# Kernel tuning notes

Hardware: AMD Instinct MI355X
Metric: run time of the kernel (lower is better)

Reference implementation:

```python
import jax, jax.numpy as jnp
import numpy as np

DIM = 1024
R = 2                      # upscale_factor
D_MODEL = DIM // (R * R)   # 256
D_INNER = 2 * D_MODEL      # expand=2 -> 512
D_STATE = 16
D_CONV = 4
DT_RANK = (D_MODEL + 15) // 16  # 16
NUM_TOKENS = 1


def pixel_shuffle(x, r):
    # (B, C*r^2, H, W) -> (B, C, H*r, W*r)
    B, C, H, W = x.shape
    c = C // (r * r)
    x = x.reshape(B, c, r, r, H, W)
    x = x.transpose(0, 1, 4, 2, 5, 3)
    return x.reshape(B, c, H * r, W * r)


def pixel_unshuffle(x, r):
    # (B, C, H*r, W*r) -> (B, C*r^2, H, W)
    B, C, Hr, Wr = x.shape
    H, W = Hr // r, Wr // r
    x = x.reshape(B, C, H, r, W, r)
    x = x.transpose(0, 1, 3, 5, 2, 4)
    return x.reshape(B, C * r * r, H, W)


def setup_inputs() -> dict:
    key = jax.random.key(0)
    ks = jax.random.split(key, 12)
    s = lambda k, shape, scale=0.02: jax.random.normal(k, shape, dtype=jnp.float32) * scale
    inp = {
        "x": jax.random.normal(ks[0], (4, DIM, 24, 24), dtype=jnp.float32),
        "global_token": jnp.zeros((1, NUM_TOKENS, D_MODEL), dtype=jnp.float32),
        "in_proj_w": s(ks[1], (2 * D_INNER, D_MODEL)),
        "conv_w": s(ks[2], (D_INNER, D_CONV), 0.1),
        "conv_b": jnp.zeros((D_INNER,), dtype=jnp.float32),
        "x_proj_w": s(ks[3], (DT_RANK + 2 * D_STATE, D_INNER)),
        "dt_proj_w": s(ks[4], (D_INNER, DT_RANK), 0.1),
        "dt_proj_b": jax.random.uniform(ks[5], (D_INNER,), dtype=jnp.float32, minval=-4.0, maxval=-2.0),
        "A_log": jnp.log(jnp.broadcast_to(jnp.arange(1, D_STATE + 1, dtype=jnp.float32), (D_INNER, D_STATE))),
        "D": jnp.ones((D_INNER,), dtype=jnp.float32),
        "out_proj_w": s(ks[6], (D_MODEL, D_INNER)),
    }
    return inp


def mamba_block(seq, in_proj_w, conv_w, conv_b, x_proj_w, dt_proj_w, dt_proj_b, A_log, D, out_proj_w):
    # seq: (B, L, d_model)
    B, L, _ = seq.shape
    xz = jnp.einsum('bld,ed->ble', seq, in_proj_w)       # (B, L, 2*d_inner)
    u, z = jnp.split(xz, 2, axis=-1)                     # each (B, L, d_inner)
    # causal depthwise conv1d (torch pad=3 + truncate to L is causal)
    up = jnp.pad(u, ((0, 0), (D_CONV - 1, 0), (0, 0)))   # left-pad time
    u = sum(up[:, k:k + L, :] * conv_w[:, k] for k in range(D_CONV)) + conv_b
    u = jax.nn.silu(u)
    x_dbl = jnp.einsum('bld,ed->ble', u, x_proj_w)
    dt, Bm, Cm = jnp.split(x_dbl, [DT_RANK, DT_RANK + D_STATE], axis=-1)
    dt = jax.nn.softplus(jnp.einsum('blr,dr->bld', dt, dt_proj_w) + dt_proj_b)  # (B,L,d_inner)
    A = -jnp.exp(A_log)                                  # (d_inner, d_state)

    def step(h, inputs):
        dt_t, B_t, C_t, u_t = inputs                     # (B,di),(B,ds),(B,ds),(B,di)
        dA = jnp.exp(dt_t[:, :, None] * A)               # (B, di, ds)
        h = dA * h + (dt_t * u_t)[:, :, None] * B_t[:, None, :]
        y = jnp.einsum('bdn,bn->bd', h, C_t)
        return h, y

    h0 = jnp.zeros((B, D_INNER, D_STATE), dtype=seq.dtype)
    xs = (dt.transpose(1, 0, 2), Bm.transpose(1, 0, 2), Cm.transpose(1, 0, 2), u.transpose(1, 0, 2))
    _, ys = jax.lax.scan(step, h0, xs)                   # (L, B, d_inner)
    y = ys.transpose(1, 0, 2) + u * D
    y = y * jax.nn.silu(z)
    return jnp.einsum('bld,ed->ble', y, out_proj_w)      # (B, L, d_model)


def reference(x, global_token, in_proj_w, conv_w, conv_b, x_proj_w, dt_proj_w, dt_proj_b, A_log, D, out_proj_w):
    B, C, H, W = x.shape
    xs = pixel_shuffle(x, R)                             # (B, d_model, 2H, 2W)
    seq = xs.reshape(B, D_MODEL, -1).transpose(0, 2, 1)  # (B, 4HW, d_model)
    tok = jnp.broadcast_to(global_token, (B, NUM_TOKENS, D_MODEL))
    seq = jnp.concatenate([tok, seq], axis=1)
    seq = mamba_block(seq, in_proj_w, conv_w, conv_b, x_proj_w, dt_proj_w, dt_proj_b, A_log, D, out_proj_w)
    seq = seq[:, -H * W * R * R:, :]                     # drop global tokens
    out = seq.reshape(B, H * R, W * R, D_MODEL).transpose(0, 3, 1, 2)
    return pixel_unshuffle(out, R)                       # (B, dim, H, W)
```

## Files before the change

kernel.cpp:

```cpp
#include <hip/hip_runtime.h>
#include <hip/hip_bf16.h>
#include <cstddef>
#include <cstdint>

#define B_ 4
#define L_ 2305
#define LSEQ 2304
#define CHUNK 32
#define NCHUNK 73
#define NC1 72
#define ML (B_*L_)

typedef __attribute__((ext_vector_type(8))) short short8;
typedef __attribute__((ext_vector_type(4))) float floatx4;

static __device__ __forceinline__ float sigmoidf_(float x){ return 1.f/(1.f+__expf(-x)); }
static __device__ __forceinline__ float softplus_(float x){
  return (x > 20.f) ? x : __logf(1.f + __expf(x));
}
static __device__ __forceinline__ float2 fma2(float2 a, float2 b, float2 c){
  return make_float2(fmaf(a.x,b.x,c.x), fmaf(a.y,b.y,c.y));
}
static __device__ __forceinline__ float2 mul2(float2 a, float2 b){
  return make_float2(a.x*b.x, a.y*b.y);
}

static __device__ __forceinline__ ushort f2bf(float v){
  __hip_bfloat16 b = __float2bfloat16(v);
  return *reinterpret_cast<ushort*>(&b);
}
static __device__ __forceinline__ float bf2f(ushort u){
  unsigned int w = ((unsigned int)u) << 16;
  return *reinterpret_cast<float*>(&w);
}
static __device__ __forceinline__ uint pack2(float2 v){
  return ((uint)f2bf(v.y) << 16) | (uint)f2bf(v.x);
}
static __device__ __forceinline__ float2 unpack2(uint w){
  return make_float2(bf2f((ushort)(w & 0xffffu)), bf2f((ushort)(w >> 16)));
}

static __device__ __forceinline__ void gload16(const void* g, void* l){
  __builtin_amdgcn_global_load_lds((const __attribute__((address_space(1))) unsigned int*)g,
                                   (__attribute__((address_space(3))) unsigned int*)l,
                                   16, 0, 0);
}

__global__ __launch_bounds__(256) void k_prep(const float* __restrict__ x,
                                              const float* __restrict__ gtok,
                                              const float* __restrict__ w_in,
                                              const float* __restrict__ w_out,
                                              const float* __restrict__ w_xp,
                                              __hip_bfloat162* __restrict__ seqb,
                                              __hip_bfloat16* __restrict__ win16,
                                              __hip_bfloat16* __restrict__ wout16,
                                              __hip_bfloat16* __restrict__ wxp16){
  int gid = blockIdx.x*256 + threadIdx.x;
  if (gid < 262144) win16[gid]  = __float2bfloat16(w_in[gid]);
  if (gid < 131072) wout16[gid] = __float2bfloat16(w_out[gid]);
  if (gid < 24576)  wxp16[gid]  = __float2bfloat16(w_xp[gid]);
  int cpair = gid & 127;
  int m = gid >> 7;
  int b = m / L_;
  int t = m - b*L_;
  int c0 = cpair << 1;
  float v0, v1;
  if (t == 0) {
    v0 = gtok[c0]; v1 = gtok[c0+1];
  } else {
    int tt = t - 1;
    int p = tt / 48, q = tt - (tt/48)*48;
    int ch0 = (c0<<2) + ((p&1)<<1) + (q&1);
    size_t base = ((size_t)(b*1024 + ch0)*24 + (p>>1))*24 + (q>>1);
    v0 = x[base];
    v1 = x[base + (size_t)4*24*24];
  }
  __hip_bfloat162 pk;
  pk.x = __float2bfloat16(v0); pk.y = __float2bfloat16(v1);
  seqb[gid] = pk;
}

__global__ __launch_bounds__(256) void k_gemm_in_mfma(const ushort* __restrict__ Aseq,
                                                      const ushort* __restrict__ W,
                                                      ushort* __restrict__ u16,
                                                      ushort* __restrict__ z16){
  __shared__ __align__(16) ushort As[2][128*32];
  __shared__ __align__(16) ushort Bs[2][128*32];
  int tid = threadIdx.x;
  int wave = tid >> 6, lane = tid & 63;
  int quad = lane >> 4, l16 = lane & 15;
  int hwlin = blockIdx.y*73 + blockIdx.x;
  int xcd = hwlin & 7, pos = hwlin >> 3;
  int logical = xcd*73 + pos;
  int row0 = (logical >> 3)*128, col0 = (logical & 7)*128;
  int wm = (wave>>1)*64, wn = (wave&1)*64;
  floatx4 acc[4][4];
  #pragma unroll
  for (int i=0;i<4;i++)
    #pragma unroll
    for (int j=0;j<4;j++)
      #pragma unroll
      for (int e=0;e<4;e++) acc[i][j][e] = 0.f;

  auto stage = [&](int buf, int k0){
    #pragma unroll
    for (int t=0;t<2;t++){
      int cid = t*256 + tid;
      int r = cid >> 2, cc = (cid & 3) << 3;
      int ar = row0 + r; if (ar > ML-1) ar = ML-1;
      gload16(Aseq + (size_t)ar*256 + k0 + cc, (char*)As[buf] + (t*256 + wave*64)*16);
      gload16(W + (size_t)(col0 + r)*256 + k0 + cc, (char*)Bs[buf] + (t*256 + wave*64)*16);
    }
  };
  auto comp = [&](int buf){
    short8 af[4], bfr[4];
    #pragma unroll
    for (int i=0;i<4;i++) af[i] = *(const short8*)(As[buf] + (wm + i*16 + l16)*32 + quad*8);
    #pragma unroll
    for (int j=0;j<4;j++) bfr[j] = *(const short8*)(Bs[buf] + (wn + j*16 + l16)*32 + quad*8);
    #pragma unroll
    for (int i=0;i<4;i++)
      #pragma unroll
      for (int j=0;j<4;j++)
        acc[i][j] = __builtin_amdgcn_mfma_f32_16x16x32_bf16(af[i], bfr[j], acc[i][j], 0, 0, 0);
  };

  stage(0, 0);
  __syncthreads();
  for (int ks = 0; ks < 7; ++ks){
    stage((ks&1)^1, (ks+1)*32);
    comp(ks&1);
    __syncthreads();
  }
  comp(1);

  #pragma unroll
  for (int i=0;i<4;i++){
    #pragma unroll
    for (int r=0;r<4;r++){
      int grow = row0 + wm + i*16 + quad*4 + r;
      if (grow < ML){
        #pragma unroll
        for (int j=0;j<4;j++){
          int gcol = col0 + wn + j*16 + l16;
          ushort v = f2bf(acc[i][j][r]);
          if (gcol < 512) u16[(size_t)grow*512 + gcol] = v;
          else            z16[(size_t)grow*512 + gcol - 512] = v;
        }
      }
    }
  }
}

__global__ __launch_bounds__(256) void k_xdbl_conv_dt(const ushort* __restrict__ U,
                                                      const ushort* __restrict__ Wx,
                                                      const float4* __restrict__ cw4,
                                                      const float*  __restrict__ cb,
                                                      const float*  __restrict__ dpw,
                                                      const float*  __restrict__ dpb,
                                                      float* __restrict__ xBC,
                                                      uint* __restrict__ dtu){
  __shared__ __align__(16) ushort Us[2][19*32];
  __shared__ __align__(16) ushort Bs[2][48*32];
  __shared__ __align__(16) ushort u_sh[16][520];
  __shared__ __align__(16) float xr[16][20];
  __shared__ __align__(16) float red[64][12];
  int tid = threadIdx.x;
  int wave = tid >> 6, lane = tid & 63;
  int quad = lane >> 4, l16 = lane & 15;
  int row0 = blockIdx.x*16;
  int myrow = row0 + l16;
  int mclamp = min(myrow, ML-1);
  int bpos = mclamp / L_;
  int lpos = mclamp - bpos*L_;
  float t3 = (lpos>=3) ? 1.f : 0.f;
  float t2 = (lpos>=2) ? 1.f : 0.f;
  float t1 = (lpos>=1) ? 1.f : 0.f;
  floatx4 acc[3];
  #pragma unroll
  for (int j=0;j<3;j++)
    #pragma unroll
    for (int e=0;e<4;e++) acc[j][e] = 0.f;

  auto stage = [&](int buf, int k0){
    if (wave == 0){
      int r = lane >> 2, cc = (lane & 3) << 3;
      int ar = min(row0 + r, ML-1);
      gload16(U + (size_t)ar*512 + k0 + cc, (char*)Us[buf] + 192);
    } else if (wave == 1){
      if (lane < 12){
        int hr = lane >> 2, hc = (lane & 3) << 3;
        int har = max(row0 - 3 + hr, 0);
        gload16(U + (size_t)har*512 + k0 + hc, (char*)Us[buf]);
      }
      int cid = 128 + lane;
      gload16(Wx + (size_t)(cid>>2)*512 + k0 + ((cid&3)<<3), (char*)Bs[buf] + 2048);
    } else {
      int cid = (wave-2)*64 + lane;
      gload16(Wx + (size_t)(cid>>2)*512 + k0 + ((cid&3)<<3), (char*)Bs[buf] + (wave-2)*1024);
    }
  };

  auto conv_mfma = [&](int buf, int k0){
    const ushort* base = Us[buf] + l16*32 + quad*8;
    short8 u0 = *(const short8*)(base);
    short8 u1 = *(const short8*)(base + 32);
    short8 u2 = *(const short8*)(base + 64);
    short8 u3 = *(const short8*)(base + 96);
    const float4* wp = cw4 + (k0 + quad*8);
    float bias[8];
    *(float4*)&bias[0] = ((const float4*)(cb + k0 + quad*8))[0];
    *(float4*)&bias[4] = ((const float4*)(cb + k0 + quad*8))[1];
    short8 af;
    uint* afp = (uint*)&af;
    float o[8];
    #pragma unroll
    for (int i=0;i<8;i++){
      float4 w = wp[i];
      float s = bias[i];
      s += (t3*w.x)*bf2f((ushort)u0[i]);
      s += (t2*w.y)*bf2f((ushort)u1[i]);
      s += (t1*w.z)*bf2f((ushort)u2[i]);
      s += (     w.w)*bf2f((ushort)u3[i]);
      o[i] = s * sigmoidf_(s);
    }
    #pragma unroll
    for (int i=0;i<4;i++) afp[i] = pack2(make_float2(o[2*i], o[2*i+1]));
    *(short8*)(&u_sh[l16][k0 + quad*8]) = af;
    #pragma unroll
    for (int j=0;j<3;j++){
      short8 bfr = *(const short8*)(Bs[buf] + (j*16 + l16)*32 + quad*8);
      acc[j] = __builtin_amdgcn_mfma_f32_16x16x32_bf16(af, bfr, acc[j], 0, 0, 0);
    }
  };

  stage(0, 0);
  __syncthreads();
  for (int ks = 0; ks < 16; ++ks){
    if (ks < 15) stage((ks&1)^1, (ks+1)*32);
    if ((ks & 3) == wave) conv_mfma(ks&1, ks*32);
    __syncthreads();
  }

  #pragma unroll
  for (int t = 1; t < 4; ++t){
    if (wave == t){
      #pragma unroll
      for (int j=0;j<3;j++)
        #pragma unroll
        for (int e=0;e<4;e++) red[lane][j*4+e] = acc[j][e];
    }
    __syncthreads();
    if (wave == 0){
      #pragma unroll
      for (int j=0;j<3;j++)
        #pragma unroll
        for (int e=0;e<4;e++) acc[j][e] += red[lane][j*4+e];
    }
    __syncthreads();
  }

  if (wave == 0){
    #pragma unroll
    for (int r=0;r<4;r++){
      int lr = quad*4 + r;
      int grow = row0 + lr;
      if (grow < ML){
        xBC[(size_t)grow*32 + l16]      = acc[1][r];
        xBC[(size_t)grow*32 + 16 + l16] = acc[2][r];
      }
      xr[lr][l16] = acc[0][r];
    }
  }
  __syncthreads();

  int d0 = tid;
  const float4* w0p = (const float4*)(dpw + ((size_t)d0 << 4));
  const float4* w1p = (const float4*)(dpw + ((size_t)(d0+256) << 4));
  float4 wa0 = w0p[0], wa1 = w0p[1], wa2 = w0p[2], wa3 = w0p[3];
  float4 wb0 = w1p[0], wb1 = w1p[1], wb2 = w1p[2], wb3 = w1p[3];
  float bias0 = dpb[d0], bias1 = dpb[d0+256];
  int mlim = min(16, ML - row0);
  for (int m = 0; m < mlim; ++m){
    const float4* xm = (const float4*)xr[m];
    float4 x0 = xm[0], x1 = xm[1], x2 = xm[2], x3 = xm[3];
    float s0 = bias0, s1 = bias1;
    s0 += wa0.x*x0.x + wa0.y*x0.y + wa0.z*x0.z + wa0.w*x0.w
        + wa1.x*x1.x + wa1.y*x1.y + wa1.z*x1.z + wa1.w*x1.w
        + wa2.x*x2.x + wa2.y*x2.y + wa2.z*x2.z + wa2.w*x2.w
        + wa3.x*x3.x + wa3.y*x3.y + wa3.z*x3.z + wa3.w*x3.w;
    s1 += wb0.x*x0.x + wb0.y*x0.y + wb0.z*x0.z + wb0.w*x0.w
        + wb1.x*x1.x + wb1.y*x1.y + wb1.z*x1.z + wb1.w*x1.w
        + wb2.x*x2.x + wb2.y*x2.y + wb2.z*x2.z + wb2.w*x2.w
        + wb3.x*x3.x + wb3.y*x3.y + wb3.z*x3.z + wb3.w*x3.w;
    size_t o = (size_t)(row0 + m)*512;
    dtu[o + d0]       = (uint)f2bf(softplus_(s0)) | ((uint)u_sh[m][d0] << 16);
    dtu[o + d0 + 256] = (uint)f2bf(softplus_(s1)) | ((uint)u_sh[m][d0+256] << 16);
  }
}

__global__ __launch_bounds__(128,4) void k_scan1(const uint* __restrict__ dtu,
                                                 const float* __restrict__ xBC,
                                                 float* __restrict__ sumdt,
                                                 ushort* __restrict__ hend16){
  __shared__ __align__(16) float Bsh[32][16];
  int c = blockIdx.x, b = blockIdx.y, qr = blockIdx.z;
  int d = (qr<<7) + threadIdx.x;
  int l0 = c*CHUNK;
  size_t off = (size_t)(b*L_ + l0)*512 + d;
  for (int i = threadIdx.x; i < 512; i += 128){
    int ll = i >> 4, n = i & 15;
    Bsh[ll][n] = xBC[(size_t)(b*L_ + l0 + ll)*32 + n];
  }
  __syncthreads();
  float2 h2[8];
  #pragma unroll
  for (int j=0;j<8;j++) h2[j] = make_float2(0.f,0.f);
  float sd = 0.f;
  #pragma unroll 4
  for (int l=0;l<32;l++){
    uint pk = dtu[off + (size_t)l*512];
    float dt = bf2f((ushort)(pk & 0xffffu));
    float u  = bf2f((ushort)(pk >> 16));
    sd += dt;
    float du = dt*u;
    float e1 = __expf(-dt);
    float e2 = e1*e1;
    float2 w = make_float2(e1,e2), ee = make_float2(e2,e2);
    float2 du2 = make_float2(du,du);
    const float4* br = (const float4*)&Bsh[l][0];
    #pragma unroll
    for (int j4=0;j4<4;j4++){
      float4 b4 = br[j4];
      h2[j4*2]   = fma2(w, h2[j4*2],   mul2(du2, make_float2(b4.x,b4.y))); w = mul2(w,ee);
      h2[j4*2+1] = fma2(w, h2[j4*2+1], mul2(du2, make_float2(b4.z,b4.w))); w = mul2(w,ee);
    }
  }
  sumdt[((c<<2)+b)*512 + d] = sd;
  uint4* hp = (uint4*)(hend16 + ((size_t)((c<<2)+b)*512 + d)*16);
  uint4 o0, o1;
  o0.x = pack2(h2[0]); o0.y = pack2(h2[1]); o0.z = pack2(h2[2]); o0.w = pack2(h2[3]);
  o1.x = pack2(h2[4]); o1.y = pack2(h2[5]); o1.z = pack2(h2[6]); o1.w = pack2(h2[7]);
  hp[0] = o0; hp[1] = o1;
}

__global__ __launch_bounds__(256) void k_scan2(const float* __restrict__ sumdt,
                                               const ushort* __restrict__ hend16,
                                               ushort* __restrict__ Hc16){
  int idx = blockIdx.x*256 + threadIdx.x;
  int n = idx & 15, d = (idx>>4) & 511, b = idx >> 13;
  float An = -(float)(n+1);
  float H = 0.f;
  #pragma unroll 4
  for (int c=0; c<NC1; c++){
    size_t base = ((size_t)((c<<2)+b)*512 + d)*16 + n;
    H = __expf(An*sumdt[((c<<2)+b)*512 + d])*H + bf2f(hend16[base]);
    Hc16[base] = f2bf(H);
  }
}

__global__ __launch_bounds__(128,4) void k_scan3(const uint* __restrict__ dtu,
                                                 const ushort* __restrict__ z16,
                                                 const float* __restrict__ xBC,
                                                 const float* __restrict__ Dp,
                                                 const ushort* __restrict__ Hc16,
                                                 __hip_bfloat16* __restrict__ y){
  __shared__ __align__(16) float BCsh[32][32];
  int c = blockIdx.x, b = blockIdx.y, qr = blockIdx.z;
  int d = (qr<<7) + threadIdx.x;
  int l0 = c*CHUNK;
  int len = min(CHUNK, L_ - l0);
  size_t off = (size_t)(b*L_ + l0)*512 + d;
  for (int i = threadIdx.x; i < 1024; i += 128){
    int ll = i >> 5, n = i & 31;
    int l = min(l0 + ll, L_-1);
    BCsh[ll][n] = xBC[(size_t)(b*L_ + l)*32 + n];
  }
  float2 h2[8];
  if (c == 0){
    #pragma unroll
    for (int j=0;j<8;j++) h2[j] = make_float2(0.f,0.f);
  } else {
    const uint4* hp = (const uint4*)(Hc16 + ((size_t)(((c-1)<<2)+b)*512 + d)*16);
    uint4 a = hp[0], bq = hp[1];
    h2[0] = unpack2(a.x);  h2[1] = unpack2(a.y);  h2[2] = unpack2(a.z);  h2[3] = unpack2(a.w);
    h2[4] = unpack2(bq.x); h2[5] = unpack2(bq.y); h2[6] = unpack2(bq.z); h2[7] = unpack2(bq.w);
  }
  float Dd = Dp[d];
  __syncthreads();
  #pragma unroll 4
  for (int l=0;l<32;l++){
    int o = min(l, len-1);
    size_t lo = off + (size_t)o*512;
    uint pk = dtu[lo];
    float dt = bf2f((ushort)(pk & 0xffffu));
    float u  = bf2f((ushort)(pk >> 16));
    float du = dt*u;
    float e1 = __expf(-dt);
    float e2 = e1*e1;
    float2 w = make_float2(e1,e2), ee = make_float2(e2,e2);
    float2 du2 = make_float2(du,du);
    float2 yacc = make_float2(0.f,0.f);
    const float4* br = (const float4*)&BCsh[l][0];
    const float4* cr = (const float4*)&BCsh[l][16];
    #pragma unroll
    for (int j4=0;j4<4;j4++){
      float4 b4 = br[j4], c4 = cr[j4];
      h2[j4*2]   = fma2(w, h2[j4*2],   mul2(du2, make_float2(b4.x,b4.y)));
      yacc       = fma2(h2[j4*2],   make_float2(c4.x,c4.y), yacc);
      w = mul2(w,ee);
      h2[j4*2+1] = fma2(w, h2[j4*2+1], mul2(du2, make_float2(b4.z,b4.w)));
      yacc       = fma2(h2[j4*2+1], make_float2(c4.z,c4.w), yacc);
      w = mul2(w,ee);
    }
    if (l < len){
      float z = bf2f(z16[lo]);
      float yo = (yacc.x + yacc.y + u*Dd) * (z * sigmoidf_(z));
      y[lo] = __float2bfloat16(yo);
    }
  }
}

__global__ __launch_bounds__(512) void k_gemm_out_mfma(const ushort* __restrict__ Y,
                                                       const ushort* __restrict__ W,
                                                       float* __restrict__ out){
  __shared__ __align__(16) ushort As[2][64*32];
  __shared__ __align__(16) ushort Bs[2][128*32];
  int tid = threadIdx.x;
  int wave = tid >> 6, lane = tid & 63;
  int quad = lane >> 4, l16 = lane & 15;
  int hwlin = blockIdx.y*144 + blockIdx.x;
  int xcd = hwlin & 7, pos = hwlin >> 3;
  int logical = xcd*36 + pos;
  int row0 = (logical >> 1)*64, col0 = (logical & 1)*128;
  int bb = row0 / LSEQ;
  int arow0 = bb*L_ + 1 + (row0 - bb*LSEQ);
  int wr = wave >> 2, wc = wave & 3;
  int wm = wr*32, wn = wc*32;
  floatx4 acc[2][2];
  #pragma unroll
  for (int i=0;i<2;i++)
    #pragma unroll
    for (int j=0;j<2;j++)
      #pragma unroll
      for (int e=0;e<2*2;e++) acc[i][j][e] = 0.f;

  auto stage = [&](int buf, int k0){
    if (wave < 4){
      int cid = wave*64 + lane;
      int r = cid >> 2, cc = (cid & 3) << 3;
      gload16(Y + (size_t)(arow0 + r)*512 + k0 + cc, (char*)As[buf] + wave*1024);
      int cid2 = 256 + cid;
      int rb = cid2 >> 2, cb2 = (cid2 & 3) << 3;
      gload16(W + (size_t)(col0 + rb)*512 + k0 + cb2, (char*)Bs[buf] + 4096 + wave*1024);
    } else {
      int cid = (wave-4)*64 + lane;
      int rb = cid >> 2, cb2 = (cid & 3) << 3;
      gload16(W + (size_t)(col0 + rb)*512 + k0 + cb2, (char*)Bs[buf] + (wave-4)*1024);
    }
  };
  auto comp = [&](int buf){
    short8 af[2], bfr[2];
    #pragma unroll
    for (int i=0;i<2;i++) af[i] = *(const short8*)(As[buf] + (wm + i*16 + l16)*32 + quad*8);
    #pragma unroll
    for (int j=0;j<2;j++) bfr[j] = *(const short8*)(Bs[buf] + (wn + j*16 + l16)*32 + quad*8);
    #pragma unroll
    for (int i=0;i<2;i++)
      #pragma unroll
      for (int j=0;j<2;j++)
        acc[i][j] = __builtin_amdgcn_mfma_f32_16x16x32_bf16(af[i], bfr[j], acc[i][j], 0, 0, 0);
  };

  stage(0, 0);
  __syncthreads();
  for (int ks = 0; ks < 15; ++ks){
    stage((ks&1)^1, (ks+1)*32);
    comp(ks&1);
    __syncthreads();
  }
  comp(1);

  #pragma unroll
  for (int i=0;i<2;i++){
    #pragma unroll
    for (int r=0;r<4;r++){
      int grow = row0 + wm + i*16 + quad*4 + r;
      int t = grow - bb*LSEQ;
      int p = t/48, q = t - (t/48)*48;
      size_t obase = (((size_t)(bb*1024) + ((p&1)<<1) + (q&1))*24 + (p>>1))*24 + (q>>1);
      #pragma unroll
      for (int j=0;j<2;j++){
        int cc = col0 + wn + j*16 + l16;
        out[obase + (size_t)cc*2304] = acc[i][j][r];
      }
    }
  }
}

extern "C" void kernel_launch(void* const* d_in, const int* in_sizes, int n_in,
                              void* d_out, int out_size, void* d_ws, size_t ws_size,
                              hipStream_t stream) {
  const float* x          = (const float*)d_in[0];
  const float* gtok       = (const float*)d_in[1];
  const float* in_proj_w  = (const float*)d_in[2];
  const float* conv_w     = (const float*)d_in[3];
  const float* conv_b     = (const float*)d_in[4];
  const float* x_proj_w   = (const float*)d_in[5];
  const float* dt_proj_w  = (const float*)d_in[6];
  const float* dt_proj_b  = (const float*)d_in[7];
  const float* A_log      = (const float*)d_in[8];
  const float* Dp         = (const float*)d_in[9];
  const float* out_proj_w = (const float*)d_in[10];
  (void)A_log;

  float* ws = (float*)d_ws;
  float* seqb_f  = ws;
  float* u16_f   = seqb_f + (size_t)ML*128;
  float* zb16_f  = u16_f  + (size_t)ML*256;
  float* dtu_f   = zb16_f + (size_t)ML*256;
  float* xBC_f   = dtu_f  + (size_t)ML*512;
  float* win16_f = xBC_f  + (size_t)ML*32;
  float* wout16_f= win16_f + 131072;
  float* wxp16_f = wout16_f + 65536;
  float* sumdt   = wxp16_f + 12288;
  float* hend_f  = sumdt + (size_t)NC1*B_*512;
  float* Hc_f    = hend_f + (size_t)NC1*B_*512*8;
  float* ybuf_f  = Hc_f   + (size_t)NC1*B_*512*8;

  __hip_bfloat16* seqb  = (__hip_bfloat16*)seqb_f;
  ushort*         ub16  = (ushort*)u16_f;
  ushort*         zb16  = (ushort*)zb16_f;
  uint*           dtu   = (uint*)dtu_f;
  __hip_bfloat16* win16 = (__hip_bfloat16*)win16_f;
  __hip_bfloat16* wout16= (__hip_bfloat16*)wout16_f;
  __hip_bfloat16* wxp16 = (__hip_bfloat16*)wxp16_f;
  ushort*         hend16= (ushort*)hend_f;
  ushort*         Hc16  = (ushort*)Hc_f;
  __hip_bfloat16* ybuf  = (__hip_bfloat16*)ybuf_f;

  k_prep        <<<4610, 256, 0, stream>>>(x, gtok, in_proj_w, out_proj_w, x_proj_w,
                                           (__hip_bfloat162*)seqb, win16, wout16, wxp16);
  k_gemm_in_mfma<<<dim3(73,8), 256, 0, stream>>>((const ushort*)seqb, (const ushort*)win16, ub16, zb16);
  k_xdbl_conv_dt<<<577, 256, 0, stream>>>(ub16, (const ushort*)wxp16, (const float4*)conv_w,
                                          conv_b, dt_proj_w, dt_proj_b, xBC_f, dtu);
  k_scan1       <<<dim3(NC1,4,4), 128, 0, stream>>>(dtu, xBC_f, sumdt, hend16);
  k_scan2       <<<128, 256, 0, stream>>>(sumdt, hend16, Hc16);
  k_scan3       <<<dim3(NCHUNK,4,4), 128, 0, stream>>>(dtu, zb16, xBC_f, Dp, Hc16, ybuf);
  k_gemm_out_mfma<<<dim3(144,2), 512, 0, stream>>>((const ushort*)ybuf, (const ushort*)wout16, (float*)d_out);
}
```

Baseline: 204.0 us.

## Replace LDS double-buffered staging in xdbl/conv kernel with direct global loads

Removes the shared-memory double-buffered staging of U rows and Wx tiles, along with the 16 per-step __syncthreads, from the fused conv+x_proj kernel. Each wave now loads its four causal-conv input rows and its B fragments straight from global memory, which is meant to cut barrier and LDS traffic overhead. In exchange it gives up software pipelining of loads. It also re-reads overlapping conv halo rows and weight rows per lane, relying on the caches for reuse.

```diff
diff --git a/kernel.cpp b/kernel.cpp
--- a/kernel.cpp
+++ b/kernel.cpp
@@ -160,8 +160,6 @@
                                                       const float*  __restrict__ dpb,
                                                       float* __restrict__ xBC,
                                                       uint* __restrict__ dtu){
-  __shared__ __align__(16) ushort Us[2][19*32];
-  __shared__ __align__(16) ushort Bs[2][48*32];
   __shared__ __align__(16) ushort u_sh[16][520];
   __shared__ __align__(16) float xr[16][20];
   __shared__ __align__(16) float red[64][12];
@@ -176,71 +174,50 @@
   float t3 = (lpos>=3) ? 1.f : 0.f;
   float t2 = (lpos>=2) ? 1.f : 0.f;
   float t1 = (lpos>=1) ? 1.f : 0.f;
+  int r3 = max(mclamp-3, 0);
+  int r2 = max(mclamp-2, 0);
+  int r1 = max(mclamp-1, 0);
   floatx4 acc[3];
   #pragma unroll
   for (int j=0;j<3;j++)
     #pragma unroll
     for (int e=0;e<4;e++) acc[j][e] = 0.f;
 
-  auto stage = [&](int buf, int k0){
-    if (wave == 0){
-      int r = lane >> 2, cc = (lane & 3) << 3;
-      int ar = min(row0 + r, ML-1);
-      gload16(U + (size_t)ar*512 + k0 + cc, (char*)Us[buf] + 192);
-    } else if (wave == 1){
-      if (lane < 12){
-        int hr = lane >> 2, hc = (lane & 3) << 3;
-        int har = max(row0 - 3 + hr, 0);
-        gload16(U + (size_t)har*512 + k0 + hc, (char*)Us[buf]);
-      }
-      int cid = 128 + lane;
-      gload16(Wx + (size_t)(cid>>2)*512 + k0 + ((cid&3)<<3), (char*)Bs[buf] + 2048);
-    } else {
-      int cid = (wave-2)*64 + lane;
-      gload16(Wx + (size_t)(cid>>2)*512 + k0 + ((cid&3)<<3), (char*)Bs[buf] + (wave-2)*1024);
-    }
-  };
-
-  auto conv_mfma = [&](int buf, int k0){
-    const ushort* base = Us[buf] + l16*32 + quad*8;
-    short8 u0 = *(const short8*)(base);
-    short8 u1 = *(const short8*)(base + 32);
-    short8 u2 = *(const short8*)(base + 64);
-    short8 u3 = *(const short8*)(base + 96);
-    const float4* wp = cw4 + (k0 + quad*8);
+  #pragma unroll
+  for (int s=0; s<4; ++s){
+    int k0 = (s*4 + wave)*32;
+    int col = k0 + quad*8;
+    short8 u0 = *(const short8*)(U + (size_t)r3*512 + col);
+    short8 u1 = *(const short8*)(U + (size_t)r2*512 + col);
+    short8 u2 = *(const short8*)(U + (size_t)r1*512 + col);
+    short8 u3 = *(const short8*)(U + (size_t)mclamp*512 + col);
+    const float4* wp = cw4 + col;
     float bias[8];
-    *(float4*)&bias[0] = ((const float4*)(cb + k0 + quad*8))[0];
-    *(float4*)&bias[4] = ((const float4*)(cb + k0 + quad*8))[1];
+    *(float4*)&bias[0] = ((const float4*)(cb + col))[0];
+    *(float4*)&bias[4] = ((const float4*)(cb + col))[1];
     short8 af;
     uint* afp = (uint*)&af;
     float o[8];
     #pragma unroll
     for (int i=0;i<8;i++){
       float4 w = wp[i];
-      float s = bias[i];
-      s += (t3*w.x)*bf2f((ushort)u0[i]);
-      s += (t2*w.y)*bf2f((ushort)u1[i]);
-      s += (t1*w.z)*bf2f((ushort)u2[i]);
-      s += (     w.w)*bf2f((ushort)u3[i]);
-      o[i] = s * sigmoidf_(s);
+      float sv = bias[i];
+      sv += (t3*w.x)*bf2f((ushort)u0[i]);
+      sv += (t2*w.y)*bf2f((ushort)u1[i]);
+      sv += (t1*w.z)*bf2f((ushort)u2[i]);
+      sv += (     w.w)*bf2f((ushort)u3[i]);
+      o[i] = sv * sigmoidf_(sv);
     }
     #pragma unroll
     for (int i=0;i<4;i++) afp[i] = pack2(make_float2(o[2*i], o[2*i+1]));
-    *(short8*)(&u_sh[l16][k0 + quad*8]) = af;
+    *(short8*)(&u_sh[l16][col]) = af;
     #pragma unroll
     for (int j=0;j<3;j++){
-      short8 bfr = *(const short8*)(Bs[buf] + (j*16 + l16)*32 + quad*8);
+      short8 bfr = *(const short8*)(Wx + (size_t)(j*16 + l16)*512 + col);
       acc[j] = __builtin_amdgcn_mfma_f32_16x16x32_bf16(af, bfr, acc[j], 0, 0, 0);
     }
-  };
-
-  stage(0, 0);
+  }
   __syncthreads();
-  for (int ks = 0; ks < 16; ++ks){
-    if (ks < 15) stage((ks&1)^1, (ks+1)*32);
-    if ((ks & 3) == wave) conv_mfma(ks&1, ks*32);
-    __syncthreads();
-  }
 
   #pragma unroll
   for (int t = 1; t < 4; ++t){
```

Result: faster. 199.6 us (median of 2 runs) (-2.1%).
